# Kernel optimization log

Hardware: AMD Instinct MI355X
Metric: run time of the kernel (lower is better)

The kernel has to match this reference:

```python
import jax, jax.numpy as jnp
import numpy as np

B, N, M, CDIM = 1024, 512, 128, 1024
OUT_DIM = 3 * M + 6  # write_lens = [M,1,1,3,1,M,M]


def setup_inputs() -> dict:
    key = jax.random.key(0)
    k1, k2, k3, k4 = jax.random.split(key, 4)
    hid = jax.random.normal(k1, (B, CDIM), dtype=jnp.float32)
    w_pre = jax.random.uniform(k2, (B, N), dtype=jnp.float32)
    w_pre = w_pre / jnp.sum(w_pre, axis=1, keepdims=True)  # valid attention dist
    memory = jax.random.normal(k3, (B, N, M), dtype=jnp.float32) * 0.1
    W_fc = jax.random.normal(k4, (OUT_DIM, CDIM), dtype=jnp.float32) / np.sqrt(CDIM)
    b_fc = jnp.zeros((OUT_DIM,), dtype=jnp.float32)
    return {"hid": hid, "w_pre": w_pre, "memory": memory, "W_fc": W_fc, "b_fc": b_fc}


def reference(hid, w_pre, memory, W_fc, b_fc):
    M_ = memory.shape[-1]
    eps = 1e-16
    # fc_write projection, split into head params
    o = hid @ W_fc.T + b_fc  # [B, 3M+6]
    bounds = np.cumsum([M_, 1, 1, 3, 1, M_])
    k, beta, g, s, gamma, e, a = jnp.split(o, bounds, axis=1)
    beta = jax.nn.softplus(beta)          # [B,1] key strength
    g = jax.nn.sigmoid(g)                 # [B,1] interpolation gate
    s = jax.nn.softmax(s, axis=1)         # [B,3] shift weights
    gamma = 1.0 + jax.nn.softplus(gamma)  # [B,1] sharpening
    e = jax.nn.sigmoid(e)                 # [B,M] erase vector

    # content addressing: cosine similarity then softmax
    mem_e = memory + eps
    k_e = k + eps
    num = jnp.einsum('bnm,bm->bn', mem_e, k_e)
    denom = jnp.linalg.norm(mem_e, axis=-1) * jnp.linalg.norm(k_e, axis=-1, keepdims=True)
    K = num / jnp.maximum(denom, 1e-8)
    wc = jax.nn.softmax(beta * K, axis=1)  # [B,N]

    # location addressing: interpolate, circular shift, sharpen
    wg = g * wc + (1.0 - g) * w_pre
    w_shift = (s[:, 0:1] * jnp.roll(wg, 1, axis=1)
               + s[:, 1:2] * wg
               + s[:, 2:3] * jnp.roll(wg, -1, axis=1))
    w_sharp = w_shift ** gamma
    w = w_sharp / (jnp.sum(w_sharp, axis=1, keepdims=True) + eps)

    # erase/add outer-product write
    mem_new = memory * (1.0 - w[:, :, None] * e[:, None, :]) + w[:, :, None] * a[:, None, :]
    return w, mem_new
```

## Files before the change

kernel.cpp:

```cpp
#include <hip/hip_runtime.h>
#include <math.h>

#define B_    1024
#define N_    512
#define M_    128
#define CDIM_ 1024
#define OUT_  390

__device__ __forceinline__ float softplus_f(float x) {
    return fmaxf(x, 0.f) + log1pf(expf(-fabsf(x)));
}
__device__ __forceinline__ float sigmoid_f(float x) {
    return 1.f / (1.f + expf(-x));
}

__global__ __launch_bounds__(256) void fc_kernel(
    const float* __restrict__ hid, const float* __restrict__ W_fc,
    const float* __restrict__ b_fc, float* __restrict__ o)
{
    __shared__ float As[32][33];
    __shared__ float Bs[32][33];
    const int tid = threadIdx.x;
    const int bm = blockIdx.x, bn = blockIdx.y;
    const int ty = tid >> 4, tx = tid & 15;

    const int lrow = tid >> 3;
    const int lcol = (tid & 7) * 4;

    float acc00 = 0.f, acc01 = 0.f, acc10 = 0.f, acc11 = 0.f;

    const int arow = bm * 32 + lrow;
    const int jrow = bn * 32 + lrow;

    for (int kc = 0; kc < CDIM_; kc += 32) {
        float4 av = *(const float4*)(hid + (size_t)arow * CDIM_ + kc + lcol);
        float4 bv = make_float4(0.f, 0.f, 0.f, 0.f);
        if (jrow < OUT_)
            bv = *(const float4*)(W_fc + (size_t)jrow * CDIM_ + kc + lcol);
        As[lrow][lcol + 0] = av.x; As[lrow][lcol + 1] = av.y;
        As[lrow][lcol + 2] = av.z; As[lrow][lcol + 3] = av.w;
        Bs[lrow][lcol + 0] = bv.x; Bs[lrow][lcol + 1] = bv.y;
        Bs[lrow][lcol + 2] = bv.z; Bs[lrow][lcol + 3] = bv.w;
        __syncthreads();
#pragma unroll
        for (int kk = 0; kk < 32; ++kk) {
            float a0 = As[ty * 2 + 0][kk];
            float a1 = As[ty * 2 + 1][kk];
            float b0 = Bs[tx * 2 + 0][kk];
            float b1 = Bs[tx * 2 + 1][kk];
            acc00 += a0 * b0; acc01 += a0 * b1;
            acc10 += a1 * b0; acc11 += a1 * b1;
        }
        __syncthreads();
    }

    const int ob = bm * 32 + ty * 2;
    const int oj = bn * 32 + tx * 2;
    if (oj < OUT_) {
        float bias0 = b_fc[oj];
        o[(size_t)(ob + 0) * OUT_ + oj] = acc00 + bias0;
        o[(size_t)(ob + 1) * OUT_ + oj] = acc10 + bias0;
    }
    if (oj + 1 < OUT_) {
        float bias1 = b_fc[oj + 1];
        o[(size_t)(ob + 0) * OUT_ + oj + 1] = acc01 + bias1;
        o[(size_t)(ob + 1) * OUT_ + oj + 1] = acc11 + bias1;
    }
}

__global__ __launch_bounds__(128) void act_kernel(
    const float* __restrict__ o,
    float* __restrict__ ws_k, float* __restrict__ ws_e,
    float* __restrict__ ws_a, float* __restrict__ params)
{
    const int b = blockIdx.x;
    const int tid = threadIdx.x;
    const float* orow = o + (size_t)b * OUT_;

    float kv = orow[tid] + 1e-16f;
    ws_k[(size_t)b * M_ + tid] = kv;

    float sq = kv * kv;
#pragma unroll
    for (int mask = 1; mask < 64; mask <<= 1) sq += __shfl_xor(sq, mask);
    __shared__ float red[2];
    if ((tid & 63) == 0) red[tid >> 6] = sq;

    float ev = sigmoid_f(orow[134 + tid]);
    ws_e[(size_t)b * M_ + tid] = ev;
    ws_a[(size_t)b * M_ + tid] = orow[262 + tid];

    __syncthreads();
    if (tid == 0) {
        float knorm = sqrtf(red[0] + red[1]);
        float beta  = softplus_f(orow[128]);
        float g     = sigmoid_f(orow[129]);
        float x0 = orow[130], x1 = orow[131], x2 = orow[132];
        float mx = fmaxf(x0, fmaxf(x1, x2));
        float e0 = expf(x0 - mx), e1 = expf(x1 - mx), e2 = expf(x2 - mx);
        float inv = 1.f / (e0 + e1 + e2);
        float gamma = 1.f + softplus_f(orow[133]);
        float* p = params + (size_t)b * 8;
        p[0] = beta; p[1] = g; p[2] = e0 * inv; p[3] = e1 * inv;
        p[4] = e2 * inv; p[5] = gamma; p[6] = knorm;
    }
}

__global__ __launch_bounds__(256) void addr_kernel(
    const float* __restrict__ memory, const float* __restrict__ w_pre,
    const float* __restrict__ ws_k, const float* __restrict__ params,
    float* __restrict__ w_out)
{
    const int b = blockIdx.x;
    const int tid = threadIdx.x;
    const int lane = tid & 63;
    const int wave = tid >> 6;

    __shared__ float k_s[M_];
    __shared__ float Ks[N_];
    __shared__ float wgs[N_];
    __shared__ float red[8];

    if (tid < M_) k_s[tid] = ws_k[(size_t)b * M_ + tid];

    const float* p = params + (size_t)b * 8;
    const float beta = p[0], g = p[1], s0 = p[2], s1 = p[3], s2 = p[4];
    const float gamma = p[5], knorm = p[6];

    __syncthreads();

    const float kd0 = k_s[lane * 2 + 0];
    const float kd1 = k_s[lane * 2 + 1];

    const float* base = memory + (size_t)b * N_ * M_ + (size_t)(wave * 128) * M_ + lane * 2;
    float2 cur = *(const float2*)(base);
    for (int i = 0; i < 128; ++i) {
        const int ip = (i < 127) ? (i + 1) : 127;
        float2 nxt = *(const float2*)(base + (size_t)ip * M_);
        float m0 = cur.x + 1e-16f;
        float m1 = cur.y + 1e-16f;
        float dot = m0 * kd0 + m1 * kd1;
        float nrm = m0 * m0 + m1 * m1;
#pragma unroll
        for (int mask = 1; mask < 64; mask <<= 1) {
            dot += __shfl_xor(dot, mask);
            nrm += __shfl_xor(nrm, mask);
        }
        if (lane == 0) {
            float denom = fmaxf(sqrtf(nrm) * knorm, 1e-8f);
            Ks[wave * 128 + i] = beta * (dot / denom);
        }
        cur = nxt;
    }
    __syncthreads();

    float v0 = Ks[tid], v1 = Ks[tid + 256];
    float mx = fmaxf(v0, v1);
#pragma unroll
    for (int mask = 1; mask < 64; mask <<= 1) mx = fmaxf(mx, __shfl_xor(mx, mask));
    if (lane == 0) red[wave] = mx;
    __syncthreads();
    mx = fmaxf(fmaxf(red[0], red[1]), fmaxf(red[2], red[3]));

    float p0 = expf(v0 - mx), p1 = expf(v1 - mx);
    float sm = p0 + p1;
#pragma unroll
    for (int mask = 1; mask < 64; mask <<= 1) sm += __shfl_xor(sm, mask);
    if (lane == 0) red[4 + wave] = sm;
    __syncthreads();
    const float inv = 1.f / (red[4] + red[5] + red[6] + red[7]);

    float wp0 = w_pre[(size_t)b * N_ + tid];
    float wp1 = w_pre[(size_t)b * N_ + tid + 256];
    float wg0 = g * (p0 * inv) + (1.f - g) * wp0;
    float wg1 = g * (p1 * inv) + (1.f - g) * wp1;
    wgs[tid] = wg0;
    wgs[tid + 256] = wg1;
    __syncthreads();

    float t0 = s0 * wgs[(tid + 511) & 511] + s1 * wgs[tid] + s2 * wgs[(tid + 1) & 511];
    int n2 = tid + 256;
    float t1 = s0 * wgs[(n2 + 511) & 511] + s1 * wgs[n2] + s2 * wgs[(n2 + 1) & 511];

    float sh0 = powf(t0, gamma);
    float sh1 = powf(t1, gamma);

    float ssum = sh0 + sh1;
#pragma unroll
    for (int mask = 1; mask < 64; mask <<= 1) ssum += __shfl_xor(ssum, mask);
    if (lane == 0) red[wave] = ssum;
    __syncthreads();
    const float winv = 1.f / (red[0] + red[1] + red[2] + red[3] + 1e-16f);

    w_out[(size_t)b * N_ + tid] = sh0 * winv;
    w_out[(size_t)b * N_ + tid + 256] = sh1 * winv;
}

__global__ __launch_bounds__(256) void write_kernel(
    const float* __restrict__ memory, const float* __restrict__ w,
    const float* __restrict__ ws_e, const float* __restrict__ ws_a,
    float* __restrict__ mem_out)
{
    const size_t idx = (size_t)blockIdx.x * 256 + threadIdx.x;
    const float4 mv = ((const float4*)memory)[idx];
    const int b   = (int)(idx >> 14);
    const int rem = (int)(idx & 16383);
    const int n   = rem >> 5;
    const int m4  = rem & 31;

    const float wv = w[(size_t)b * N_ + n];
    const float4 ev = ((const float4*)ws_e)[(size_t)b * 32 + m4];
    const float4 av = ((const float4*)ws_a)[(size_t)b * 32 + m4];

    float4 ov;
    ov.x = mv.x * (1.f - wv * ev.x) + wv * av.x;
    ov.y = mv.y * (1.f - wv * ev.y) + wv * av.y;
    ov.z = mv.z * (1.f - wv * ev.z) + wv * av.z;
    ov.w = mv.w * (1.f - wv * ev.w) + wv * av.w;
    ((float4*)mem_out)[idx] = ov;
}

extern "C" void kernel_launch(void* const* d_in, const int* in_sizes, int n_in,
                              void* d_out, int out_size, void* d_ws, size_t ws_size,
                              hipStream_t stream)
{
    const float* hid    = (const float*)d_in[0];
    const float* w_pre  = (const float*)d_in[1];
    const float* memory = (const float*)d_in[2];
    const float* W_fc   = (const float*)d_in[3];
    const float* b_fc   = (const float*)d_in[4];

    float* out     = (float*)d_out;
    float* w_out   = out;
    float* mem_out = out + (size_t)B_ * N_;

    float* ws     = (float*)d_ws;
    float* o      = ws;
    float* ws_k   = o    + (size_t)B_ * OUT_;
    float* ws_e   = ws_k + (size_t)B_ * M_;
    float* ws_a   = ws_e + (size_t)B_ * M_;
    float* params = ws_a + (size_t)B_ * M_;

    dim3 g1(B_ / 32, (OUT_ + 31) / 32);
    fc_kernel<<<g1, 256, 0, stream>>>(hid, W_fc, b_fc, o);
    act_kernel<<<B_, 128, 0, stream>>>(o, ws_k, ws_e, ws_a, params);
    addr_kernel<<<B_, 256, 0, stream>>>(memory, w_pre, ws_k, params, w_out);

    const int total4 = B_ * N_ * M_ / 4;
    write_kernel<<<total4 / 256, 256, 0, stream>>>(memory, w_out, ws_e, ws_a, mem_out);
}
```

Measured before the change: 569.6 us.

## Fuse addressing and memory write, vectorize similarity loop, split-K FC GEMM

Merges the addressing and erase/add write kernels so each block rereads its memory slice right after computing weights, with e/a/w held in shared memory. The cosine-similarity loop now uses float4 loads across 16-lane groups with shorter shuffle reductions instead of full-wave reductions per row. The FC projection becomes a split-K GEMM with 64x64 tiles and 4x4 register blocking, and bias plus partial sums are reduced in the activation kernel. This trades an extra partial-sum buffer and relies on cache hits for the second memory read.

After: 521.3 us. -8.5%, faster.

```diff
diff --git a/kernel.cpp b/kernel.cpp
--- a/kernel.cpp
+++ b/kernel.cpp
@@ -6,6 +6,9 @@
 #define M_    128
 #define CDIM_ 1024
 #define OUT_  390
+#define OUTP_ 448
+#define SPLITK 4
+#define KCH   (CDIM_ / SPLITK)
 
 __device__ __forceinline__ float softplus_f(float x) {
     return fmaxf(x, 0.f) + log1pf(expf(-fabsf(x)));
@@ -16,112 +19,142 @@
 
 __global__ __launch_bounds__(256) void fc_kernel(
     const float* __restrict__ hid, const float* __restrict__ W_fc,
-    const float* __restrict__ b_fc, float* __restrict__ o)
-{
-    __shared__ float As[32][33];
-    __shared__ float Bs[32][33];
+    float* __restrict__ part)
+{
+    __shared__ float As[16][68];
+    __shared__ float Bs[16][68];
+
     const int tid = threadIdx.x;
-    const int bm = blockIdx.x, bn = blockIdx.y;
-    const int ty = tid >> 4, tx = tid & 15;
-
-    const int lrow = tid >> 3;
-    const int lcol = (tid & 7) * 4;
-
-    float acc00 = 0.f, acc01 = 0.f, acc10 = 0.f, acc11 = 0.f;
-
-    const int arow = bm * 32 + lrow;
-    const int jrow = bn * 32 + lrow;
-
-    for (int kc = 0; kc < CDIM_; kc += 32) {
-        float4 av = *(const float4*)(hid + (size_t)arow * CDIM_ + kc + lcol);
+    const int bm = blockIdx.x, bn = blockIdx.y, bk = blockIdx.z;
+    const int rb = bm * 64;
+    const int jb = bn * 64;
+    const int kb = bk * KCH;
+
+    const int tx = tid & 15;
+    const int ty = tid >> 4;
+
+    const int srow = tid >> 2;
+    const int scol = (tid & 3) * 4;
+
+    const int arow = rb + srow;
+    const int jrow = jb + srow;
+    const bool jvalid = (jrow < OUT_);
+
+    float acc[4][4];
+#pragma unroll
+    for (int r = 0; r < 4; ++r)
+#pragma unroll
+        for (int c = 0; c < 4; ++c) acc[r][c] = 0.f;
+
+    for (int kt = 0; kt < KCH; kt += 16) {
+        float4 av = *(const float4*)(hid + (size_t)arow * CDIM_ + kb + kt + scol);
         float4 bv = make_float4(0.f, 0.f, 0.f, 0.f);
-        if (jrow < OUT_)
-            bv = *(const float4*)(W_fc + (size_t)jrow * CDIM_ + kc + lcol);
-        As[lrow][lcol + 0] = av.x; As[lrow][lcol + 1] = av.y;
-        As[lrow][lcol + 2] = av.z; As[lrow][lcol + 3] = av.w;
-        Bs[lrow][lcol + 0] = bv.x; Bs[lrow][lcol + 1] = bv.y;
-        Bs[lrow][lcol + 2] = bv.z; Bs[lrow][lcol + 3] = bv.w;
+        if (jvalid)
+            bv = *(const float4*)(W_fc + (size_t)jrow * CDIM_ + kb + kt + scol);
+        As[scol + 0][srow] = av.x; As[scol + 1][srow] = av.y;
+        As[scol + 2][srow] = av.z; As[scol + 3][srow] = av.w;
+        Bs[scol + 0][srow] = bv.x; Bs[scol + 1][srow] = bv.y;
+        Bs[scol + 2][srow] = bv.z; Bs[scol + 3][srow] = bv.w;
         __syncthreads();
 #pragma unroll
-        for (int kk = 0; kk < 32; ++kk) {
-            float a0 = As[ty * 2 + 0][kk];
-            float a1 = As[ty * 2 + 1][kk];
-            float b0 = Bs[tx * 2 + 0][kk];
-            float b1 = Bs[tx * 2 + 1][kk];
-            acc00 += a0 * b0; acc01 += a0 * b1;
-            acc10 += a1 * b0; acc11 += a1 * b1;
+        for (int k = 0; k < 16; ++k) {
+            float4 a = *(const float4*)&As[k][ty * 4];
+            float4 b = *(const float4*)&Bs[k][tx * 4];
+            float ar[4] = {a.x, a.y, a.z, a.w};
+            float br[4] = {b.x, b.y, b.z, b.w};
+#pragma unroll
+            for (int r = 0; r < 4; ++r)
+#pragma unroll
+                for (int c = 0; c < 4; ++c)
+                    acc[r][c] += ar[r] * br[c];
         }
         __syncthreads();
     }
 
-    const int ob = bm * 32 + ty * 2;
-    const int oj = bn * 32 + tx * 2;
-    if (oj < OUT_) {
-        float bias0 = b_fc[oj];
-        o[(size_t)(ob + 0) * OUT_ + oj] = acc00 + bias0;
-        o[(size_t)(ob + 1) * OUT_ + oj] = acc10 + bias0;
-    }
-    if (oj + 1 < OUT_) {
-        float bias1 = b_fc[oj + 1];
-        o[(size_t)(ob + 0) * OUT_ + oj + 1] = acc01 + bias1;
-        o[(size_t)(ob + 1) * OUT_ + oj + 1] = acc11 + bias1;
+    float* pbase = part + (size_t)bk * B_ * OUTP_;
+#pragma unroll
+    for (int r = 0; r < 4; ++r) {
+        float4 v = make_float4(acc[r][0], acc[r][1], acc[r][2], acc[r][3]);
+        *(float4*)(pbase + (size_t)(rb + ty * 4 + r) * OUTP_ + jb + tx * 4) = v;
     }
 }
 
 __global__ __launch_bounds__(128) void act_kernel(
-    const float* __restrict__ o,
+    const float* __restrict__ part, const float* __restrict__ b_fc,
     float* __restrict__ ws_k, float* __restrict__ ws_e,
     float* __restrict__ ws_a, float* __restrict__ params)
 {
     const int b = blockIdx.x;
     const int tid = threadIdx.x;
-    const float* orow = o + (size_t)b * OUT_;
-
-    float kv = orow[tid] + 1e-16f;
-    ws_k[(size_t)b * M_ + tid] = kv;
-
-    float sq = kv * kv;
+    const float* pb = part + (size_t)b * OUTP_;
+    const size_t S = (size_t)B_ * OUTP_;
+
+    float vk = b_fc[tid];
+    float ve = b_fc[134 + tid];
+    float va = b_fc[262 + tid];
+#pragma unroll
+    for (int s = 0; s < SPLITK; ++s) {
+        vk += pb[s * S + tid];
+        ve += pb[s * S + 134 + tid];
+        va += pb[s * S + 262 + tid];
+    }
+    vk += 1e-16f;
+    ws_k[(size_t)b * M_ + tid] = vk;
+    ws_e[(size_t)b * M_ + tid] = sigmoid_f(ve);
+    ws_a[(size_t)b * M_ + tid] = va;
+
+    float sq = vk * vk;
 #pragma unroll
     for (int mask = 1; mask < 64; mask <<= 1) sq += __shfl_xor(sq, mask);
     __shared__ float red[2];
+    __shared__ float sscal[6];
     if ((tid & 63) == 0) red[tid >> 6] = sq;
-
-    float ev = sigmoid_f(orow[134 + tid]);
-    ws_e[(size_t)b * M_ + tid] = ev;
-    ws_a[(size_t)b * M_ + tid] = orow[262 + tid];
-
+    if (tid < 6) {
+        float v = b_fc[128 + tid];
+#pragma unroll
+        for (int s = 0; s < SPLITK; ++s) v += pb[s * S + 128 + tid];
+        sscal[tid] = v;
+    }
     __syncthreads();
     if (tid == 0) {
         float knorm = sqrtf(red[0] + red[1]);
-        float beta  = softplus_f(orow[128]);
-        float g     = sigmoid_f(orow[129]);
-        float x0 = orow[130], x1 = orow[131], x2 = orow[132];
+        float beta  = softplus_f(sscal[0]);
+        float g     = sigmoid_f(sscal[1]);
+        float x0 = sscal[2], x1 = sscal[3], x2 = sscal[4];
         float mx = fmaxf(x0, fmaxf(x1, x2));
         float e0 = expf(x0 - mx), e1 = expf(x1 - mx), e2 = expf(x2 - mx);
         float inv = 1.f / (e0 + e1 + e2);
-        float gamma = 1.f + softplus_f(orow[133]);
+        float gamma = 1.f + softplus_f(sscal[5]);
         float* p = params + (size_t)b * 8;
         p[0] = beta; p[1] = g; p[2] = e0 * inv; p[3] = e1 * inv;
         p[4] = e2 * inv; p[5] = gamma; p[6] = knorm;
     }
 }
 
-__global__ __launch_bounds__(256) void addr_kernel(
+__global__ __launch_bounds__(256) void addr_write_kernel(
     const float* __restrict__ memory, const float* __restrict__ w_pre,
-    const float* __restrict__ ws_k, const float* __restrict__ params,
-    float* __restrict__ w_out)
+    const float* __restrict__ ws_k, const float* __restrict__ ws_e,
+    const float* __restrict__ ws_a, const float* __restrict__ params,
+    float* __restrict__ w_out, float* __restrict__ mem_out)
 {
     const int b = blockIdx.x;
     const int tid = threadIdx.x;
     const int lane = tid & 63;
     const int wave = tid >> 6;
 
-    __shared__ float k_s[M_];
+    __shared__ __align__(16) float k_s[M_];
+    __shared__ __align__(16) float e_s[M_];
+    __shared__ __align__(16) float a_s[M_];
     __shared__ float Ks[N_];
     __shared__ float wgs[N_];
+    __shared__ float ws_f[N_];
     __shared__ float red[8];
 
-    if (tid < M_) k_s[tid] = ws_k[(size_t)b * M_ + tid];
+    if (tid < M_) {
+        k_s[tid] = ws_k[(size_t)b * M_ + tid];
+        e_s[tid] = ws_e[(size_t)b * M_ + tid];
+        a_s[tid] = ws_a[(size_t)b * M_ + tid];
+    }
 
     const float* p = params + (size_t)b * 8;
     const float beta = p[0], g = p[1], s0 = p[2], s1 = p[3], s2 = p[4];
@@ -129,28 +162,36 @@
 
     __syncthreads();
 
-    const float kd0 = k_s[lane * 2 + 0];
-    const float kd1 = k_s[lane * 2 + 1];
-
-    const float* base = memory + (size_t)b * N_ * M_ + (size_t)(wave * 128) * M_ + lane * 2;
-    float2 cur = *(const float2*)(base);
-    for (int i = 0; i < 128; ++i) {
-        const int ip = (i < 127) ? (i + 1) : 127;
-        float2 nxt = *(const float2*)(base + (size_t)ip * M_);
-        float m0 = cur.x + 1e-16f;
-        float m1 = cur.y + 1e-16f;
-        float dot = m0 * kd0 + m1 * kd1;
-        float nrm = m0 * m0 + m1 * m1;
-#pragma unroll
-        for (int mask = 1; mask < 64; mask <<= 1) {
+    const int sub = lane >> 4;
+    const int j16 = lane & 15;
+    float kd[8];
+#pragma unroll
+    for (int t = 0; t < 8; ++t) kd[t] = k_s[j16 * 8 + t];
+
+    const float* mb = memory + (size_t)b * N_ * M_;
+#pragma unroll 2
+    for (int i = 0; i < 32; ++i) {
+        const int n = wave * 128 + i * 4 + sub;
+        const float* rowp = mb + (size_t)n * M_ + j16 * 8;
+        float4 x0 = *(const float4*)(rowp);
+        float4 x1 = *(const float4*)(rowp + 4);
+        float xv[8] = {x0.x, x0.y, x0.z, x0.w, x1.x, x1.y, x1.z, x1.w};
+        float dot = 0.f, nrm = 0.f;
+#pragma unroll
+        for (int t = 0; t < 8; ++t) {
+            float m = xv[t] + 1e-16f;
+            dot += m * kd[t];
+            nrm += m * m;
+        }
+#pragma unroll
+        for (int mask = 1; mask < 16; mask <<= 1) {
             dot += __shfl_xor(dot, mask);
             nrm += __shfl_xor(nrm, mask);
         }
-        if (lane == 0) {
+        if (j16 == 0) {
             float denom = fmaxf(sqrtf(nrm) * knorm, 1e-8f);
-            Ks[wave * 128 + i] = beta * (dot / denom);
-        }
-        cur = nxt;
+            Ks[n] = beta * (dot / denom);
+        }
     }
     __syncthreads();
 
@@ -179,7 +220,7 @@
     __syncthreads();
 
     float t0 = s0 * wgs[(tid + 511) & 511] + s1 * wgs[tid] + s2 * wgs[(tid + 1) & 511];
-    int n2 = tid + 256;
+    const int n2 = tid + 256;
     float t1 = s0 * wgs[(n2 + 511) & 511] + s1 * wgs[n2] + s2 * wgs[(n2 + 1) & 511];
 
     float sh0 = powf(t0, gamma);
@@ -192,32 +233,34 @@
     __syncthreads();
     const float winv = 1.f / (red[0] + red[1] + red[2] + red[3] + 1e-16f);
 
-    w_out[(size_t)b * N_ + tid] = sh0 * winv;
-    w_out[(size_t)b * N_ + tid + 256] = sh1 * winv;
-}
-
-__global__ __launch_bounds__(256) void write_kernel(
-    const float* __restrict__ memory, const float* __restrict__ w,
-    const float* __restrict__ ws_e, const float* __restrict__ ws_a,
-    float* __restrict__ mem_out)
-{
-    const size_t idx = (size_t)blockIdx.x * 256 + threadIdx.x;
-    const float4 mv = ((const float4*)memory)[idx];
-    const int b   = (int)(idx >> 14);
-    const int rem = (int)(idx & 16383);
-    const int n   = rem >> 5;
-    const int m4  = rem & 31;
-
-    const float wv = w[(size_t)b * N_ + n];
-    const float4 ev = ((const float4*)ws_e)[(size_t)b * 32 + m4];
-    const float4 av = ((const float4*)ws_a)[(size_t)b * 32 + m4];
-
-    float4 ov;
-    ov.x = mv.x * (1.f - wv * ev.x) + wv * av.x;
-    ov.y = mv.y * (1.f - wv * ev.y) + wv * av.y;
-    ov.z = mv.z * (1.f - wv * ev.z) + wv * av.z;
-    ov.w = mv.w * (1.f - wv * ev.w) + wv * av.w;
-    ((float4*)mem_out)[idx] = ov;
+    float wf0 = sh0 * winv;
+    float wf1 = sh1 * winv;
+    w_out[(size_t)b * N_ + tid] = wf0;
+    w_out[(size_t)b * N_ + tid + 256] = wf1;
+    ws_f[tid] = wf0;
+    ws_f[tid + 256] = wf1;
+    __syncthreads();
+
+    const float4* min4 = (const float4*)(mb);
+    float4* mout4 = (float4*)(mem_out + (size_t)b * N_ * M_);
+    const float4* e4 = (const float4*)e_s;
+    const float4* a4 = (const float4*)a_s;
+#pragma unroll 2
+    for (int i = 0; i < 64; ++i) {
+        const int idx = i * 256 + tid;
+        const int n   = idx >> 5;
+        const int m4  = idx & 31;
+        float4 mv = min4[idx];
+        float wv = ws_f[n];
+        float4 ev = e4[m4];
+        float4 av = a4[m4];
+        float4 ov;
+        ov.x = mv.x * (1.f - wv * ev.x) + wv * av.x;
+        ov.y = mv.y * (1.f - wv * ev.y) + wv * av.y;
+        ov.z = mv.z * (1.f - wv * ev.z) + wv * av.z;
+        ov.w = mv.w * (1.f - wv * ev.w) + wv * av.w;
+        mout4[idx] = ov;
+    }
 }
 
 extern "C" void kernel_launch(void* const* d_in, const int* in_sizes, int n_in,
@@ -235,17 +278,15 @@
     float* mem_out = out + (size_t)B_ * N_;
 
     float* ws     = (float*)d_ws;
-    float* o      = ws;
-    float* ws_k   = o    + (size_t)B_ * OUT_;
+    float* part   = ws;
+    float* ws_k   = part + (size_t)SPLITK * B_ * OUTP_;
     float* ws_e   = ws_k + (size_t)B_ * M_;
     float* ws_a   = ws_e + (size_t)B_ * M_;
     float* params = ws_a + (size_t)B_ * M_;
 
-    dim3 g1(B_ / 32, (OUT_ + 31) / 32);
-    fc_kernel<<<g1, 256, 0, stream>>>(hid, W_fc, b_fc, o);
-    act_kernel<<<B_, 128, 0, stream>>>(o, ws_k, ws_e, ws_a, params);
-    addr_kernel<<<B_, 256, 0, stream>>>(memory, w_pre, ws_k, params, w_out);
-
-    const int total4 = B_ * N_ * M_ / 4;
-    write_kernel<<<total4 / 256, 256, 0, stream>>>(memory, w_out, ws_e, ws_a, mem_out);
-}
+    dim3 g1(B_ / 64, OUTP_ / 64, SPLITK);
+    fc_kernel<<<g1, 256, 0, stream>>>(hid, W_fc, part);
+    act_kernel<<<B_, 128, 0, stream>>>(part, b_fc, ws_k, ws_e, ws_a, params);
+    addr_write_kernel<<<B_, 256, 0, stream>>>(memory, w_pre, ws_k, ws_e, ws_a,
+                                              params, w_out, mem_out);
+}
```
